# Optimization experiments

Hardware: AMD Instinct MI355X
Metric: run time of the kernel (lower is better)

## Reference

```python
import jax, jax.numpy as jnp
import numpy as np

OUT = 14      # RoIAlign output size
RATIO = 2     # sampling ratio per bin
NMS_THR = 0.5


def _pairwise_iou(b):
    # b: [N,4] xyxy
    x1, y1, x2, y2 = b[:, 0], b[:, 1], b[:, 2], b[:, 3]
    area = (x2 - x1) * (y2 - y1)
    ix1 = jnp.maximum(x1[:, None], x1[None, :])
    iy1 = jnp.maximum(y1[:, None], y1[None, :])
    ix2 = jnp.minimum(x2[:, None], x2[None, :])
    iy2 = jnp.minimum(y2[:, None], y2[None, :])
    inter = jnp.clip(ix2 - ix1, 0.0) * jnp.clip(iy2 - iy1, 0.0)
    return inter / (area[:, None] + area[None, :] - inter + 1e-9)


def _nms(verts, scores, level, thr):
    # greedy NMS restricted to boxes assigned to the same FPN level
    N = verts.shape[0]
    order = jnp.argsort(-scores)
    bs, ls = verts[order], level[order]
    iou = _pairwise_iou(bs)
    idx = jnp.arange(N)
    sup_mat = (iou > thr) & (ls[:, None] == ls[None, :]) & (idx[None, :] > idx[:, None])
    def body(i, keep):
        return keep & ~(sup_mat[i] & keep[i])
    keep_s = jax.lax.fori_loop(0, N, body, jnp.ones((N,), dtype=bool))
    return jnp.zeros((N,), dtype=bool).at[order].set(keep_s)


def _roi_align(feat, rois):
    # feat: [C,H,W]; rois: [N,4] xyxy in feature-map coords
    C, H, W = feat.shape
    N = rois.shape[0]
    S = OUT * RATIO
    x1, y1, x2, y2 = rois[:, 0], rois[:, 1], rois[:, 2], rois[:, 3]
    bw = (x2 - x1) / OUT
    bh = (y2 - y1) / OUT
    g = (jnp.arange(S, dtype=feat.dtype) + 0.5) / RATIO  # sample grid in bin units
    sx = x1[:, None] + g[None, :] * bw[:, None]           # [N,S]
    sy = y1[:, None] + g[None, :] * bh[:, None]
    xs = jnp.broadcast_to(jnp.clip(sx, 0.0, W - 1.0)[:, None, :], (N, S, S))
    ys = jnp.broadcast_to(jnp.clip(sy, 0.0, H - 1.0)[:, :, None], (N, S, S))
    x0 = jnp.floor(xs); y0 = jnp.floor(ys)
    x0i = x0.astype(jnp.int32); y0i = y0.astype(jnp.int32)
    x1i = jnp.minimum(x0i + 1, W - 1)
    y1i = jnp.minimum(y0i + 1, H - 1)
    lx = xs - x0; ly = ys - y0
    flat = feat.reshape(C, H * W)
    def gather(yi, xi):
        return jnp.take(flat, (yi * W + xi).reshape(-1), axis=1).reshape(C, N, S, S)
    v = (gather(y0i, x0i) * (1 - ly) * (1 - lx)
         + gather(y0i, x1i) * (1 - ly) * lx
         + gather(y1i, x0i) * ly * (1 - lx)
         + gather(y1i, x1i) * ly * lx)
    # average the RATIO x RATIO samples per output bin
    v = v.reshape(C, N, OUT, RATIO, OUT, RATIO).mean(axis=(3, 5))
    return jnp.transpose(v, (1, 0, 2, 3))  # [N,C,14,14]


def reference(p4, p8, p16, p32, boxes, scores):
    # boxes: [B,N,4] (cx,cy,w,h) in image coords; scores: [B,N]
    w, h = boxes[..., 2], boxes[..., 3]
    # FPN level assignment: clamp(floor(3 + log2(sqrt(w*h)/224)), 1, 4)
    level = jnp.clip(jnp.floor(3.0 + jnp.log2(jnp.sqrt(w * h) / 224.0)), 1.0, 4.0)
    cx, cy = boxes[..., 0], boxes[..., 1]
    verts = jnp.stack([cx - w / 2, cy - h / 2, cx + w / 2, cy + h / 2], axis=-1)
    keep = jax.vmap(lambda v, s, l: _nms(v, s, l, NMS_THR))(verts, scores, level)
    feats = {1: p4, 2: p8, 3: p16, 4: p32}
    pooled = jnp.zeros(boxes.shape[:2] + (p4.shape[1], OUT, OUT), dtype=p4.dtype)
    for l in (1, 2, 3, 4):
        stride = float(2 * 2 ** l)  # 4/8/16/32, matches prepare_boxes
        p = jax.vmap(_roi_align)(feats[l], verts / stride)  # [B,N,C,14,14]
        sel = ((level == l) & keep)[:, :, None, None, None]
        pooled = pooled + jnp.where(sel, p, 0.0)
    out_boxes = jnp.where(keep[..., None], verts, 0.0)
    return pooled, out_boxes, keep


def setup_inputs() -> dict:
    key = jax.random.key(0)
    ks = jax.random.split(key, 7)
    B, N, C = 2, 512, 256
    p4 = jax.random.normal(ks[0], (B, C, 256, 256), jnp.float32)
    p8 = jax.random.normal(ks[1], (B, C, 128, 128), jnp.float32)
    p16 = jax.random.normal(ks[2], (B, C, 64, 64), jnp.float32)
    p32 = jax.random.normal(ks[3], (B, C, 32, 32), jnp.float32)
    cxcy = jax.random.uniform(ks[4], (B, N, 2), jnp.float32) * 1024.0
    wh = 16.0 + jax.random.uniform(ks[5], (B, N, 2), jnp.float32) * 496.0
    boxes = jnp.concatenate([cxcy, wh], axis=-1)
    scores = jax.random.uniform(ks[6], (B, N), jnp.float32)
    return {"p4": p4, "p8": p8, "p16": p16, "p32": p32, "boxes": boxes, "scores": scores}
```

## Files before the change

kernel.cpp:

```cpp
#include <hip/hip_runtime.h>

#define NB 2
#define NN 512
#define NC 256
#define OUTP 14
#define SS 28
#define CH_SPLIT 4
#define CH_PER_BLK (NC / CH_SPLIT)
#define ELEMS_PER_BLK (CH_PER_BLK * OUTP * OUTP)
#define POOL_PER_BOX (NC * OUTP * OUTP)
#define POOL_TOTAL (NB * NN * POOL_PER_BOX)
#define BOX_OFF POOL_TOTAL
#define KEEP_OFF (POOL_TOTAL + NB * NN * 4)

#define CPW 16
#define PATCH_MAX 1256

typedef const __attribute__((address_space(1))) unsigned int GU32;
typedef __attribute__((address_space(3))) unsigned int LU32;

__global__ __launch_bounds__(512) void k_nms(const float* __restrict__ boxes,
                                             const float* __restrict__ scores,
                                             float* __restrict__ dout) {
    int b = blockIdx.x;
    int tid = threadIdx.x;
    __shared__ float sS[NN];
    __shared__ int sI[NN];
    __shared__ float4 sB[NN];
    __shared__ float sA[NN];
    __shared__ int sL[NN];
    __shared__ unsigned long long sup[NN][8];
    __shared__ unsigned long long skw[8];
    __shared__ int korig[NN];

    sS[tid] = scores[b * NN + tid];
    sI[tid] = tid;
    __syncthreads();
    for (int k = 2; k <= NN; k <<= 1) {
        for (int j = k >> 1; j > 0; j >>= 1) {
            int ixj = tid ^ j;
            if (ixj > tid) {
                float s1 = sS[tid], s2 = sS[ixj];
                int i1 = sI[tid], i2 = sI[ixj];
                bool lt = (s1 > s2) || (s1 == s2 && i1 < i2);
                bool up = ((tid & k) == 0);
                if (up ? !lt : lt) {
                    sS[tid] = s2; sS[ixj] = s1;
                    sI[tid] = i2; sI[ixj] = i1;
                }
            }
            __syncthreads();
        }
    }
    {
        int o = sI[tid];
        float4 bx = ((const float4*)boxes)[b * NN + o];
        float w = bx.z, h = bx.w;
        float x1 = bx.x - w * 0.5f, y1 = bx.y - h * 0.5f;
        float x2 = bx.x + w * 0.5f, y2 = bx.y + h * 0.5f;
        float s = sqrtf(w * h);
        int lvl = (s < 112.f) ? 1 : ((s < 224.f) ? 2 : ((s < 448.f) ? 3 : 4));
        sB[tid] = make_float4(x1, y1, x2, y2);
        sA[tid] = (x2 - x1) * (y2 - y1);
        sL[tid] = lvl;
    }
    __syncthreads();
    {
        float4 bi = sB[tid];
        float areai = sA[tid];
        int il = sL[tid];
        for (int cg = 0; cg < 8; ++cg) {
            unsigned long long m = 0ull;
            int jb = cg << 6;
#pragma unroll 4
            for (int k = 0; k < 64; ++k) {
                int j = jb + k;
                float4 bj = sB[j];
                float xx1 = fmaxf(bi.x, bj.x);
                float yy1 = fmaxf(bi.y, bj.y);
                float xx2 = fminf(bi.z, bj.z);
                float yy2 = fminf(bi.w, bj.w);
                float inter = fmaxf(xx2 - xx1, 0.0f) * fmaxf(yy2 - yy1, 0.0f);
                float denom = areai + sA[j] - inter + 1e-9f;
                bool sp = (j > tid) && (sL[j] == il) && ((inter / denom) > 0.5f);
                m |= sp ? (1ull << k) : 0ull;
            }
            sup[tid][cg] = m;
        }
    }
    __syncthreads();
    if (tid < 64) {
        int myw = tid & 7;
        unsigned long long kwl = ~0ull;
        for (int w = 0; w < 8; ++w) {
            unsigned long long aw = __shfl(kwl, w);
            int ibase = w << 6;
            for (int bb = 0; bb < 64; ++bb) {
                int i = ibase + bb;
                unsigned long long rw = sup[i][w];
                unsigned long long rl = sup[i][myw];
                if ((aw >> bb) & 1ull) {
                    aw &= ~rw;
                    kwl &= ~rl;
                }
            }
        }
        if (tid < 8) skw[tid] = kwl;
    }
    __syncthreads();
    korig[sI[tid]] = (int)((skw[tid >> 6] >> (tid & 63)) & 1ull);
    __syncthreads();
    {
        float4 bx = ((const float4*)boxes)[b * NN + tid];
        float kf = korig[tid] ? 1.0f : 0.0f;
        float x1 = (bx.x - bx.z * 0.5f) * kf;
        float y1 = (bx.y - bx.w * 0.5f) * kf;
        float x2 = (bx.x + bx.z * 0.5f) * kf;
        float y2 = (bx.y + bx.w * 0.5f) * kf;
        ((float4*)(dout + BOX_OFF))[b * NN + tid] = make_float4(x1, y1, x2, y2);
        dout[KEEP_OFF + b * NN + tid] = kf;
    }
}

__global__ __launch_bounds__(256) void k_roi(const float* __restrict__ p4,
                                             const float* __restrict__ p8,
                                             const float* __restrict__ p16,
                                             const float* __restrict__ p32,
                                             const float* __restrict__ boxes,
                                             float* __restrict__ dout) {
    int blk = blockIdx.x;
    int box = blk >> 2;
    int chunk = blk & 3;
    int b = box >> 9;
    int tid = threadIdx.x;
    float* obase = dout + (size_t)box * POOL_PER_BOX + (size_t)chunk * ELEMS_PER_BLK;
    float keepf = dout[KEEP_OFF + box];
    if (keepf < 0.5f) {
        float4 z = make_float4(0.f, 0.f, 0.f, 0.f);
        float4* o4 = (float4*)obase;
        for (int i = tid; i < ELEMS_PER_BLK / 4; i += 256) o4[i] = z;
        return;
    }
    float4 bx = ((const float4*)boxes)[box];
    float w = bx.z, h = bx.w;
    float s = sqrtf(w * h);
    int lvl = (s < 112.f) ? 0 : ((s < 224.f) ? 1 : ((s < 448.f) ? 2 : 3));
    const float* feat = (lvl == 0) ? p4 : ((lvl == 1) ? p8 : ((lvl == 2) ? p16 : p32));
    int HW = 256 >> lvl;
    float inv = 1.0f / (float)(4 << lvl);
    int planesz = HW * HW;
    const float* plane0 = feat + (size_t)b * NC * planesz + (size_t)(chunk * CH_PER_BLK) * planesz;

    float x1r = (bx.x - w * 0.5f) * inv;
    float bwr = w * inv / 14.0f;
    float y1r = (bx.y - h * 0.5f) * inv;
    float bhr = h * inv / 14.0f;
    float hwm1 = (float)(HW - 1);
    float xs_first = fminf(fmaxf(x1r + 0.25f * bwr, 0.0f), hwm1);
    float xs_last  = fminf(fmaxf(x1r + 13.75f * bwr, 0.0f), hwm1);
    float ys_first = fminf(fmaxf(y1r + 0.25f * bhr, 0.0f), hwm1);
    float ys_last  = fminf(fmaxf(y1r + 13.75f * bhr, 0.0f), hwm1);
    int x_lo = min((int)floorf(xs_first), HW - 2);
    int x_hi = min((int)floorf(xs_last) + 1, HW - 1);
    int y_lo = min((int)floorf(ys_first), HW - 2);
    int y_hi = min((int)floorf(ys_last) + 1, HW - 1);
    int PW = x_hi - x_lo + 1;
    int PH = y_hi - y_lo + 1;
    int cells = PW * PH;
    int cm1 = cells - 1;
    float invPW = 1.0f / (float)PW;
    int I64 = (cells + 63) >> 6;

    __shared__ float patch[4][2][PATCH_MAX];
    __shared__ int sXc0[SS], sYoff[SS];
    __shared__ float sLX[SS], sLY[SS];

    if (tid < SS) {
        float g = (tid + 0.5f) * 0.5f;
        float xs = fminf(fmaxf(x1r + g * bwr, 0.0f), hwm1);
        int x0 = min((int)floorf(xs), HW - 2);
        sXc0[tid] = x0 - x_lo;
        sLX[tid] = xs - (float)x0;
        float ys = fminf(fmaxf(y1r + g * bhr, 0.0f), hwm1);
        int y0 = min((int)floorf(ys), HW - 2);
        sYoff[tid] = (y0 - y_lo) * PW;
        sLY[tid] = ys - (float)y0;
    }
    __syncthreads();

    int wid = tid >> 6;
    int lane = tid & 63;
    const int base_gidx = y_lo * HW + x_lo;
    const float* wplane = plane0 + (size_t)(wid * CPW) * planesz + base_gidx;
    float* wout = obase + (size_t)(wid * CPW) * 196;
    LU32* wlds0 = (LU32*)&patch[wid][0][0];
    LU32* wlds1 = (LU32*)&patch[wid][1][0];

#define STAGE(j, ldsp)                                                                      \
    do {                                                                                    \
        const float* pl_ = wplane + (size_t)(j) * planesz;                                  \
        for (int k_ = 0; k_ < I64; ++k_) {                                                  \
            int i_ = lane + (k_ << 6);                                                      \
            int iq_ = min(i_, cm1);                                                         \
            int row_ = (int)(((float)iq_ + 0.5f) * invPW);                                  \
            int voff_ = row_ * (HW - PW) + iq_;                           \
            __builtin_amdgcn_global_load_lds((GU32*)(pl_ + voff_), (ldsp) + i_, 4, 0, 0);   \
        }                                                                                   \
    } while (0)

#define VMCNT(N) asm volatile("s_waitcnt vmcnt(" #N ")" ::: "memory")

    STAGE(0, wlds0);

    for (int j = 0; j < CPW; ++j) {
        if (j + 1 < CPW) {
            STAGE(j + 1, (j & 1) ? wlds0 : wlds1);
            switch (I64) {
                case 1:  VMCNT(1);  break;
                case 2:  VMCNT(2);  break;
                case 3:  VMCNT(3);  break;
                case 4:  VMCNT(4);  break;
                case 5:  VMCNT(5);  break;
                case 6:  VMCNT(6);  break;
                case 7:  VMCNT(7);  break;
                case 8:  VMCNT(8);  break;
                case 9:  VMCNT(9);  break;
                case 10: VMCNT(10); break;
                case 11: VMCNT(11); break;
                case 12: VMCNT(12); break;
                case 13: VMCNT(13); break;
                case 14: VMCNT(14); break;
                case 15: VMCNT(15); break;
                default: VMCNT(16); break;
            }
        } else {
            VMCNT(0);
        }

        const float* P = &patch[wid][j & 1][0];
        float* oc = wout + j * 196;
#pragma unroll
        for (int it = 0; it < 2; ++it) {
            int p0 = (lane << 1) + (it << 7);
            if (p0 < 196) {
                int py = p0 / 14;
                int px = p0 - py * 14;
                int iy = py << 1;
                int ro0 = sYoff[iy],  ro1 = sYoff[iy + 1];
                float ly0 = sLY[iy],  ly1 = sLY[iy + 1];
                float2 r;
#pragma unroll
                for (int q = 0; q < 2; ++q) {
                    int ix = (px + q) << 1;
                    int c00 = sXc0[ix],   c01 = sXc0[ix + 1];
                    float lx0 = sLX[ix],  lx1 = sLX[ix + 1];
                    float acc = 0.f;
#define SAMPLE(RO, LY, CC, LX)                                        \
                    {                                                 \
                        const float* q_ = P + (RO) + (CC);            \
                        float f00 = q_[0], f01 = q_[1];               \
                        const float* q2_ = q_ + PW;                   \
                        float f10 = q2_[0], f11 = q2_[1];             \
                        float top = f00 + (LX) * (f01 - f00);         \
                        float bot = f10 + (LX) * (f11 - f10);         \
                        acc += top + (LY) * (bot - top);              \
                    }
                    SAMPLE(ro0, ly0, c00, lx0)
                    SAMPLE(ro0, ly0, c01, lx1)
                    SAMPLE(ro1, ly1, c00, lx0)
                    SAMPLE(ro1, ly1, c01, lx1)
#undef SAMPLE
                    if (q == 0) r.x = acc * 0.25f; else r.y = acc * 0.25f;
                }
                *(float2*)(oc + p0) = r;
            }
        }
    }
#undef STAGE
#undef VMCNT
}

extern "C" void kernel_launch(void* const* d_in, const int* in_sizes, int n_in,
                              void* d_out, int out_size, void* d_ws, size_t ws_size,
                              hipStream_t stream) {
    const float* p4 = (const float*)d_in[0];
    const float* p8 = (const float*)d_in[1];
    const float* p16 = (const float*)d_in[2];
    const float* p32 = (const float*)d_in[3];
    const float* boxes = (const float*)d_in[4];
    const float* scores = (const float*)d_in[5];
    float* out = (float*)d_out;

    k_nms<<<NB, NN, 0, stream>>>(boxes, scores, out);
    k_roi<<<NB * NN * CH_SPLIT, 256, 0, stream>>>(p4, p8, p16, p32, boxes, out);
}
```

Baseline: 539.7 us.

## Share one double-buffered patch across a 128-thread block for all chunk channels

The RoIAlign kernel moves from 256-thread blocks, where each wave stages its own private double-buffered patch for 16 channels, to 128-thread blocks. Both waves now cooperatively stage a single shared patch per channel and iterate over all 64 channels in the chunk, with block barriers around each buffer swap. The aim is to cut LDS use per block sharply so more blocks fit per CU, improving occupancy and latency hiding. The cost is two barriers per channel and a smaller patch buffer, which could overflow for unusually large patches.

```diff
diff --git a/kernel.cpp b/kernel.cpp
--- a/kernel.cpp
+++ b/kernel.cpp
@@ -13,8 +13,7 @@
 #define BOX_OFF POOL_TOTAL
 #define KEEP_OFF (POOL_TOTAL + NB * NN * 4)
 
-#define CPW 16
-#define PATCH_MAX 1256
+#define PATCH_MAX 1152
 
 typedef const __attribute__((address_space(1))) unsigned int GU32;
 typedef __attribute__((address_space(3))) unsigned int LU32;
@@ -122,12 +121,12 @@
     }
 }
 
-__global__ __launch_bounds__(256) void k_roi(const float* __restrict__ p4,
-                                             const float* __restrict__ p8,
-                                             const float* __restrict__ p16,
-                                             const float* __restrict__ p32,
-                                             const float* __restrict__ boxes,
-                                             float* __restrict__ dout) {
+__global__ __launch_bounds__(128, 8) void k_roi(const float* __restrict__ p4,
+                                                const float* __restrict__ p8,
+                                                const float* __restrict__ p16,
+                                                const float* __restrict__ p32,
+                                                const float* __restrict__ boxes,
+                                                float* __restrict__ dout) {
     int blk = blockIdx.x;
     int box = blk >> 2;
     int chunk = blk & 3;
@@ -138,7 +137,7 @@
     if (keepf < 0.5f) {
         float4 z = make_float4(0.f, 0.f, 0.f, 0.f);
         float4* o4 = (float4*)obase;
-        for (int i = tid; i < ELEMS_PER_BLK / 4; i += 256) o4[i] = z;
+        for (int i = tid; i < ELEMS_PER_BLK / 4; i += 128) o4[i] = z;
         return;
     }
     float4 bx = ((const float4*)boxes)[box];
@@ -169,9 +168,9 @@
     int cells = PW * PH;
     int cm1 = cells - 1;
     float invPW = 1.0f / (float)PW;
-    int I64 = (cells + 63) >> 6;
-
-    __shared__ float patch[4][2][PATCH_MAX];
+    int I = (cells + 127) >> 7;
+
+    __shared__ float patch[2][PATCH_MAX];
     __shared__ int sXc0[SS], sYoff[SS];
     __shared__ float sLX[SS], sLY[SS];
 
@@ -186,36 +185,32 @@
         sYoff[tid] = (y0 - y_lo) * PW;
         sLY[tid] = ys - (float)y0;
     }
-    __syncthreads();
-
-    int wid = tid >> 6;
-    int lane = tid & 63;
+
     const int base_gidx = y_lo * HW + x_lo;
-    const float* wplane = plane0 + (size_t)(wid * CPW) * planesz + base_gidx;
-    float* wout = obase + (size_t)(wid * CPW) * 196;
-    LU32* wlds0 = (LU32*)&patch[wid][0][0];
-    LU32* wlds1 = (LU32*)&patch[wid][1][0];
-
-#define STAGE(j, ldsp)                                                                      \
+    const float* wplane = plane0 + base_gidx;
+    const int hwmpw = HW - PW;
+
+#define STAGE(j, bufi)                                                                      \
     do {                                                                                    \
         const float* pl_ = wplane + (size_t)(j) * planesz;                                  \
-        for (int k_ = 0; k_ < I64; ++k_) {                                                  \
-            int i_ = lane + (k_ << 6);                                                      \
+        LU32* dst_ = (LU32*)&patch[bufi][0];                                                \
+        for (int k_ = 0; k_ < I; ++k_) {                                                    \
+            int i_ = tid + (k_ << 7);                                                       \
             int iq_ = min(i_, cm1);                                                         \
             int row_ = (int)(((float)iq_ + 0.5f) * invPW);                                  \
-            int voff_ = row_ * (HW - PW) + iq_;                           \
-            __builtin_amdgcn_global_load_lds((GU32*)(pl_ + voff_), (ldsp) + i_, 4, 0, 0);   \
+            int voff_ = row_ * hwmpw + iq_;                               \
+            __builtin_amdgcn_global_load_lds((GU32*)(pl_ + voff_), dst_ + i_, 4, 0, 0);     \
         }                                                                                   \
     } while (0)
 
 #define VMCNT(N) asm volatile("s_waitcnt vmcnt(" #N ")" ::: "memory")
 
-    STAGE(0, wlds0);
-
-    for (int j = 0; j < CPW; ++j) {
-        if (j + 1 < CPW) {
-            STAGE(j + 1, (j & 1) ? wlds0 : wlds1);
-            switch (I64) {
+    STAGE(0, 0);
+
+    for (int j = 0; j < CH_PER_BLK; ++j) {
+        if (j + 1 < CH_PER_BLK) {
+            STAGE(j + 1, (j + 1) & 1);
+            switch (I) {
                 case 1:  VMCNT(1);  break;
                 case 2:  VMCNT(2);  break;
                 case 3:  VMCNT(3);  break;
@@ -224,56 +219,54 @@
                 case 6:  VMCNT(6);  break;
                 case 7:  VMCNT(7);  break;
                 case 8:  VMCNT(8);  break;
-                case 9:  VMCNT(9);  break;
-                case 10: VMCNT(10); break;
-                case 11: VMCNT(11); break;
-                case 12: VMCNT(12); break;
-                case 13: VMCNT(13); break;
-                case 14: VMCNT(14); break;
-                case 15: VMCNT(15); break;
-                default: VMCNT(16); break;
+                default: VMCNT(9);  break;
             }
         } else {
             VMCNT(0);
         }
-
-        const float* P = &patch[wid][j & 1][0];
-        float* oc = wout + j * 196;
+        __builtin_amdgcn_s_barrier();
+        asm volatile("" ::: "memory");
+
+        const float* P = &patch[j & 1][0];
+        float* oc = obase + j * 196;
+        if (tid < 98) {
+            int p0 = tid << 1;
+            int py = p0 / 14;
+            int px = p0 - py * 14;
+            int iy = py << 1;
+            int ro0 = sYoff[iy],  ro1 = sYoff[iy + 1];
+            float ly0 = sLY[iy],  ly1 = sLY[iy + 1];
+            float2 r;
 #pragma unroll
-        for (int it = 0; it < 2; ++it) {
-            int p0 = (lane << 1) + (it << 7);
-            if (p0 < 196) {
-                int py = p0 / 14;
-                int px = p0 - py * 14;
-                int iy = py << 1;
-                int ro0 = sYoff[iy],  ro1 = sYoff[iy + 1];
-                float ly0 = sLY[iy],  ly1 = sLY[iy + 1];
-                float2 r;
-#pragma unroll
-                for (int q = 0; q < 2; ++q) {
-                    int ix = (px + q) << 1;
-                    int c00 = sXc0[ix],   c01 = sXc0[ix + 1];
-                    float lx0 = sLX[ix],  lx1 = sLX[ix + 1];
-                    float acc = 0.f;
+            for (int q = 0; q < 2; ++q) {
+                int ix = (px + q) << 1;
+                int c00 = sXc0[ix],   c01 = sXc0[ix + 1];
+                float lx0 = sLX[ix],  lx1 = sLX[ix + 1];
+                float acc = 0.f;
 #define SAMPLE(RO, LY, CC, LX)                                        \
-                    {                                                 \
-                        const float* q_ = P + (RO) + (CC);            \
-                        float f00 = q_[0], f01 = q_[1];               \
-                        const float* q2_ = q_ + PW;                   \
-                        float f10 = q2_[0], f11 = q2_[1];             \
-                        float top = f00 + (LX) * (f01 - f00);         \
-                        float bot = f10 + (LX) * (f11 - f10);         \
-                        acc += top + (LY) * (bot - top);              \
-                    }
-                    SAMPLE(ro0, ly0, c00, lx0)
-                    SAMPLE(ro0, ly0, c01, lx1)
-                    SAMPLE(ro1, ly1, c00, lx0)
-                    SAMPLE(ro1, ly1, c01, lx1)
+                {                                                     \
+                    const float* q_ = P + (RO) + (CC);                \
+                    float f00 = q_[0], f01 = q_[1];                   \
+                    const float* q2_ = q_ + PW;                       \
+                    float f10 = q2_[0], f11 = q2_[1];                 \
+                    float top = f00 + (LX) * (f01 - f00);             \
+                    float bot = f10 + (LX) * (f11 - f10);             \
+                    acc += top + (LY) * (bot - top);                  \
+                }
+                SAMPLE(ro0, ly0, c00, lx0)
+                SAMPLE(ro0, ly0, c01, lx1)
+                SAMPLE(ro1, ly1, c00, lx0)
+                SAMPLE(ro1, ly1, c01, lx1)
 #undef SAMPLE
-                    if (q == 0) r.x = acc * 0.25f; else r.y = acc * 0.25f;
-                }
-                *(float2*)(oc + p0) = r;
-            }
+                if (q == 0) r.x = acc * 0.25f; else r.y = acc * 0.25f;
+            }
+            *(float2*)(oc + p0) = r;
+        }
+
+        if (j + 1 < CH_PER_BLK) {
+            asm volatile("" ::: "memory");
+            __builtin_amdgcn_s_barrier();
+            asm volatile("" ::: "memory");
         }
     }
 #undef STAGE
@@ -292,5 +285,5 @@
     float* out = (float*)d_out;
 
     k_nms<<<NB, NN, 0, stream>>>(boxes, scores, out);
-    k_roi<<<NB * NN * CH_SPLIT, 256, 0, stream>>>(p4, p8, p16, p32, boxes, out);
+    k_roi<<<NB * NN * CH_SPLIT, 128, 0, stream>>>(p4, p8, p16, p32, boxes, out);
 }
```

New measurement: 553.8 us. +2.6%, slower.
